# Kernel tuning notes

Hardware: AMD Instinct MI355X
Metric: run time of the kernel (lower is better)

Reference implementation:

```python
import jax, jax.numpy as jnp
import numpy as np

N_NODES = 50000
N_EDGES = 640000
DIM = 128
N_LAYERS = 4
K_MAX = 4


def setup_inputs() -> dict:
    key = jax.random.key(0)
    k1, k2, k3, k4, k5, k6 = jax.random.split(key, 6)
    x = jax.random.normal(k1, (N_NODES, DIM), dtype=jnp.float32)
    edge_index = jax.random.randint(k2, (2, N_EDGES), 0, N_NODES, dtype=jnp.int32)
    edge_attr = jax.random.randint(k3, (N_EDGES,), 1, K_MAX + 1, dtype=jnp.int32)  # hop k in [1, k_max]
    W = jax.random.normal(k4, (N_LAYERS, DIM, DIM), dtype=jnp.float32) * 0.05
    b = jax.random.normal(k5, (N_LAYERS, DIM), dtype=jnp.float32) * 0.01
    alpha = jax.random.normal(k6, (N_LAYERS, K_MAX), dtype=jnp.float32)
    return {"x": x, "edge_index": edge_index, "edge_attr": edge_attr,
            "W": W, "b": b, "alpha": alpha}


def reference(x, edge_index, edge_attr, W, b, alpha):
    # SP-GCN stage: per-hop GCN convs with shared per-layer weight W[t],
    # combined with softmax(alpha[t]) hop weights, residual + ReLU + L2 norm.
    N, D = x.shape
    L, K = alpha.shape
    src, dst = edge_index[0], edge_index[1]
    k_idx = edge_attr - 1                              # [E] in [0, K)

    # Per-(node, hop) in-degree with self-loop (+1), as in gcn_norm per k-subgraph.
    seg = dst * K + k_idx
    ones = jnp.ones(src.shape[0], dtype=x.dtype)
    deg = jax.ops.segment_sum(ones, seg, num_segments=N * K).reshape(N, K) + 1.0  # [N, K]
    dinv = jax.lax.rsqrt(deg)
    # symmetric norm per edge within its hop-k subgraph
    norm_e = dinv[src, k_idx] * dinv[dst, k_idx]       # [E]

    for t in range(L):
        a = jax.nn.softmax(alpha[t])                   # [K] hop weights
        h = x @ W[t]                                   # [N, D]
        # sum_k alpha_k * conv_k fused: per-edge weight alpha[k_e] * norm_e
        msg = (a[k_idx] * norm_e)[:, None] * h[src]    # [E, D]
        agg = jax.ops.segment_sum(msg, dst, num_segments=N)
        # self-loop contributions: sum_k alpha_k / deg[n, k]
        self_coef = jnp.sum(a[None, :] / deg, axis=1)  # [N]
        out = agg + self_coef[:, None] * h + b[t]
        x = x + jax.nn.relu(out)
        # F.normalize(p=2, dim=-1), eps=1e-12
        nrm = jnp.maximum(jnp.linalg.norm(x, axis=-1, keepdims=True), 1e-12)
        x = x / nrm
    return x
```

## Files before the change

### kernel.cpp

```cpp
#include <hip/hip_runtime.h>
#include <hip/hip_fp16.h>
#include <math.h>

#define DIM 128
#define KH 4

typedef unsigned int uint;
typedef unsigned short ushort;
using short8v = __attribute__((ext_vector_type(8))) short;
using f32x4 = __attribute__((ext_vector_type(4))) float;

__device__ __forceinline__ uint f2bf(float f) {
  uint u = __float_as_uint(f);
  return (u + 0x7fffu + ((u >> 16) & 1u)) >> 16;
}
__device__ __forceinline__ float bf2f(uint u) { return __uint_as_float(u << 16); }
__device__ __forceinline__ float bflo(uint u) { return __uint_as_float(u << 16); }
__device__ __forceinline__ float bfhi(uint u) { return __uint_as_float(u & 0xffff0000u); }

__global__ __launch_bounds__(256) void k_init_count(
    const float4* __restrict__ xin, float4* __restrict__ X4,
    uint* __restrict__ Xhi, uint* __restrict__ Xlo,
    const int* __restrict__ ei, const int* __restrict__ attr,
    uint* __restrict__ degpack, int n4, int E) {
  int i = blockIdx.x * 256 + threadIdx.x;
  if (i < n4) {
    float4 v = xin[i];
    X4[i] = v;
    uint h0 = f2bf(v.x), h1 = f2bf(v.y), h2 = f2bf(v.z), h3 = f2bf(v.w);
    Xhi[i * 2 + 0] = h0 | (h1 << 16);
    Xhi[i * 2 + 1] = h2 | (h3 << 16);
    uint l0 = f2bf(v.x - bf2f(h0)), l1 = f2bf(v.y - bf2f(h1));
    uint l2 = f2bf(v.z - bf2f(h2)), l3 = f2bf(v.w - bf2f(h3));
    Xlo[i * 2 + 0] = l0 | (l1 << 16);
    Xlo[i * 2 + 1] = l2 | (l3 << 16);
  }
  if (i < E) {
    int dst = ei[E + i];
    int k = attr[i] - 1;
    atomicAdd(&degpack[dst], 1u << (k * 8));
  }
}

__global__ __launch_bounds__(256) void k_scan1(const uint* __restrict__ degpack,
                                               int* __restrict__ off,
                                               int* __restrict__ bsum, int n) {
  __shared__ int s[256];
  int t = threadIdx.x;
  int i = blockIdx.x * 256 + t;
  int v = 0;
  if (i < n) {
    uint w = degpack[i];
    v = (w & 0xff) + ((w >> 8) & 0xff) + ((w >> 16) & 0xff) + (w >> 24);
  }
  s[t] = v;
  __syncthreads();
  for (int d = 1; d < 256; d <<= 1) {
    int u = (t >= d) ? s[t - d] : 0;
    __syncthreads();
    s[t] += u;
    __syncthreads();
  }
  if (i < n) off[i] = s[t] - v;
  if (t == 255) bsum[blockIdx.x] = s[255];
}

__global__ __launch_bounds__(256) void k_scan2(const int* __restrict__ bsum,
                                               int* __restrict__ bex, int nb) {
  __shared__ int s[256];
  int t = threadIdx.x;
  int v = (t < nb) ? bsum[t] : 0;
  s[t] = v;
  __syncthreads();
  for (int d = 1; d < 256; d <<= 1) {
    int u = (t >= d) ? s[t - d] : 0;
    __syncthreads();
    s[t] += u;
    __syncthreads();
  }
  if (t < nb) bex[t] = s[t] - v;
}

__global__ __launch_bounds__(256) void k_scan3w(int* __restrict__ off,
                                                const int* __restrict__ bex,
                                                const uint* __restrict__ degpack,
                                                int* __restrict__ cursor4,
                                                float* __restrict__ dinv, int n,
                                                const float* __restrict__ W,
                                                short* __restrict__ Whi,
                                                short* __restrict__ Wlo, int wtot) {
  int i = blockIdx.x * 256 + threadIdx.x;
  if (i < n) {
    int o = off[i] + bex[blockIdx.x];
    off[i] = o;
    uint w = degpack[i];
    int b0 = w & 0xff, b1 = (w >> 8) & 0xff, b2 = (w >> 16) & 0xff, b3 = w >> 24;
    int4 c;
    c.x = o;
    c.y = o + b0;
    c.z = o + b0 + b1;
    c.w = o + b0 + b1 + b2;
    *(int4*)&cursor4[i * 4] = c;
    float4 dv;
    dv.x = rsqrtf((float)b0 + 1.0f);
    dv.y = rsqrtf((float)b1 + 1.0f);
    dv.z = rsqrtf((float)b2 + 1.0f);
    dv.w = rsqrtf((float)b3 + 1.0f);
    *(float4*)&dinv[i * 4] = dv;
  }
  if (i < wtot) {
    int l = i >> 14;
    int rem = i & 16383;
    int k = rem >> 7;
    int ncol = rem & 127;
    float w = W[i];
    uint h = f2bf(w);
    uint lo = f2bf(w - bf2f(h));
    size_t o = (size_t)l * 16384 + (size_t)ncol * 128 + k;
    Whi[o] = (short)h;
    Wlo[o] = (short)lo;
  }
}

__global__ __launch_bounds__(256) void k_scatter(const int* __restrict__ ei,
                                                 const int* __restrict__ attr,
                                                 const float* __restrict__ dinv,
                                                 int* __restrict__ cursor4,
                                                 uint* __restrict__ srcnm, int E) {
  int e = blockIdx.x * 256 + threadIdx.x;
  if (e >= E) return;
  int src = ei[e];
  int dst = ei[E + e];
  int k = attr[e] - 1;
  float nm = dinv[src * KH + k] * dinv[dst * KH + k];
  ushort h = __half_as_ushort(__float2half(nm));
  int pos = atomicAdd(&cursor4[dst * KH + k], 1);
  srcnm[pos] = (uint)src | ((uint)h << 16);
}

__global__ __launch_bounds__(512) void k_gemm(const uint* __restrict__ Xhi,
                                              const uint* __restrict__ Xlo,
                                              const short* __restrict__ Whi,
                                              const short* __restrict__ Wlo,
                                              ushort* __restrict__ Hb16, int N) {
  __shared__ __align__(16) short xs_hi[64 * 128];
  __shared__ __align__(16) short xs_lo[64 * 128];
  int t = threadIdx.x;
  int r0 = blockIdx.x * 64;

#pragma unroll
  for (int i = 0; i < 2; ++i) {
    int fi = i * 512 + t;
    int row = fi >> 4, kq = fi & 15;
    int rg = r0 + row;
    if (rg >= N) rg = N - 1;
    int swz = kq ^ (row & 7);
    *(uint4*)&xs_hi[row * 128 + swz * 8] = *(const uint4*)&Xhi[(size_t)rg * 64 + kq * 4];
    *(uint4*)&xs_lo[row * 128 + swz * 8] = *(const uint4*)&Xlo[(size_t)rg * 64 + kq * 4];
  }
  __syncthreads();

  int wid = t >> 6, lane = t & 63;
  int wrow = wid & 1, wcol = wid >> 1;
  int lr = lane & 15, lk = lane >> 4;

  f32x4 acc[2][2];
#pragma unroll
  for (int a = 0; a < 2; ++a)
#pragma unroll
    for (int c = 0; c < 2; ++c) acc[a][c] = (f32x4){0.f, 0.f, 0.f, 0.f};

#pragma unroll
  for (int ks = 0; ks < 4; ++ks) {
    int k0 = ks * 32 + lk * 8;
    short8v ah[2], al[2];
#pragma unroll
    for (int rt = 0; rt < 2; ++rt) {
      int r = wrow * 32 + rt * 16 + lr;
      int slot = (k0 >> 3) ^ (r & 7);
      ah[rt] = *(short8v*)&xs_hi[r * 128 + slot * 8];
      al[rt] = *(short8v*)&xs_lo[r * 128 + slot * 8];
    }
    short8v bh[2], bl[2];
#pragma unroll
    for (int ct = 0; ct < 2; ++ct) {
      int col = wcol * 32 + ct * 16 + lr;
      bh[ct] = *(const short8v*)&Whi[(size_t)col * 128 + k0];
      bl[ct] = *(const short8v*)&Wlo[(size_t)col * 128 + k0];
    }
#pragma unroll
    for (int rt = 0; rt < 2; ++rt)
#pragma unroll
      for (int ct = 0; ct < 2; ++ct) {
        acc[rt][ct] = __builtin_amdgcn_mfma_f32_16x16x32_bf16(ah[rt], bh[ct], acc[rt][ct], 0, 0, 0);
        acc[rt][ct] = __builtin_amdgcn_mfma_f32_16x16x32_bf16(al[rt], bh[ct], acc[rt][ct], 0, 0, 0);
        acc[rt][ct] = __builtin_amdgcn_mfma_f32_16x16x32_bf16(ah[rt], bl[ct], acc[rt][ct], 0, 0, 0);
      }
  }

#pragma unroll
  for (int rt = 0; rt < 2; ++rt)
#pragma unroll
    for (int ct = 0; ct < 2; ++ct) {
      int col = wcol * 32 + ct * 16 + lr;
#pragma unroll
      for (int i = 0; i < 4; ++i) {
        int row = r0 + wrow * 32 + rt * 16 + lk * 4 + i;
        if (row < N) Hb16[(size_t)row * 128 + col] = (ushort)f2bf(acc[rt][ct][i]);
      }
    }
}

__global__ __launch_bounds__(256) void k_agg(const int* __restrict__ off,
                                             const uint* __restrict__ degpack,
                                             const uint* __restrict__ srcnm,
                                             const float* __restrict__ dinv,
                                             const uint* __restrict__ Hb,
                                             const float* __restrict__ bias,
                                             const float* __restrict__ alpha,
                                             float* __restrict__ X,
                                             uint* __restrict__ Xhi,
                                             uint* __restrict__ Xlo, int N) {
  int wid = threadIdx.x >> 6;
  int lane = threadIdx.x & 63;
  int n = blockIdx.x * 4 + wid;
  if (n >= N) return;

  float a0 = alpha[0], a1 = alpha[1], a2 = alpha[2], a3 = alpha[3];
  float m = fmaxf(fmaxf(a0, a1), fmaxf(a2, a3));
  a0 = __expf(a0 - m); a1 = __expf(a1 - m); a2 = __expf(a2 - m); a3 = __expf(a3 - m);
  float is = 1.0f / (a0 + a1 + a2 + a3);
  a0 *= is; a1 *= is; a2 *= is; a3 *= is;

  uint w = degpack[n];
  int b0 = w & 0xff, b1 = (w >> 8) & 0xff, b2 = (w >> 16) & 0xff, b3 = (int)(w >> 24);
  int e0 = off[n];
  int e1 = e0 + b0 + b1 + b2 + b3;
  int k1 = e0 + b0, k2 = k1 + b1, k3 = k2 + b2;

  float accx = 0.f, accy = 0.f;

  for (int base = e0; base < e1; base += 64) {
    int cnt = min(64, e1 - base);
    int sofs = 0;
    float wc = 0.f;
    if (lane < cnt) {
      uint v = srcnm[base + lane];
      int pos = base + lane;
      int k = (pos >= k1) + (pos >= k2) + (pos >= k3);
      float ak = (k == 0) ? a0 : (k == 1) ? a1 : (k == 2) ? a2 : a3;
      wc = ak * __half2float(__ushort_as_half((ushort)(v >> 16)));
      sofs = (int)(v & 0xFFFFu) << 6;
    }
    int j = 0;
    for (; j + 8 <= cnt; j += 8) {
      int s0 = __shfl(sofs, j),     s1 = __shfl(sofs, j + 1);
      int s2 = __shfl(sofs, j + 2), s3 = __shfl(sofs, j + 3);
      int s4 = __shfl(sofs, j + 4), s5 = __shfl(sofs, j + 5);
      int s6 = __shfl(sofs, j + 6), s7 = __shfl(sofs, j + 7);
      float w0 = __shfl(wc, j),     w1 = __shfl(wc, j + 1);
      float w2 = __shfl(wc, j + 2), w3 = __shfl(wc, j + 3);
      float w4 = __shfl(wc, j + 4), w5 = __shfl(wc, j + 5);
      float w6 = __shfl(wc, j + 6), w7 = __shfl(wc, j + 7);
      uint u0 = Hb[s0 + lane];
      uint u1 = Hb[s1 + lane];
      uint u2 = Hb[s2 + lane];
      uint u3 = Hb[s3 + lane];
      uint u4 = Hb[s4 + lane];
      uint u5 = Hb[s5 + lane];
      uint u6 = Hb[s6 + lane];
      uint u7 = Hb[s7 + lane];
      accx = fmaf(w0, bflo(u0), accx); accy = fmaf(w0, bfhi(u0), accy);
      accx = fmaf(w1, bflo(u1), accx); accy = fmaf(w1, bfhi(u1), accy);
      accx = fmaf(w2, bflo(u2), accx); accy = fmaf(w2, bfhi(u2), accy);
      accx = fmaf(w3, bflo(u3), accx); accy = fmaf(w3, bfhi(u3), accy);
      accx = fmaf(w4, bflo(u4), accx); accy = fmaf(w4, bfhi(u4), accy);
      accx = fmaf(w5, bflo(u5), accx); accy = fmaf(w5, bfhi(u5), accy);
      accx = fmaf(w6, bflo(u6), accx); accy = fmaf(w6, bfhi(u6), accy);
      accx = fmaf(w7, bflo(u7), accx); accy = fmaf(w7, bfhi(u7), accy);
    }
    for (; j + 4 <= cnt; j += 4) {
      int s0 = __shfl(sofs, j),     s1 = __shfl(sofs, j + 1);
      int s2 = __shfl(sofs, j + 2), s3 = __shfl(sofs, j + 3);
      float w0 = __shfl(wc, j),     w1 = __shfl(wc, j + 1);
      float w2 = __shfl(wc, j + 2), w3 = __shfl(wc, j + 3);
      uint u0 = Hb[s0 + lane];
      uint u1 = Hb[s1 + lane];
      uint u2 = Hb[s2 + lane];
      uint u3 = Hb[s3 + lane];
      accx = fmaf(w0, bflo(u0), accx); accy = fmaf(w0, bfhi(u0), accy);
      accx = fmaf(w1, bflo(u1), accx); accy = fmaf(w1, bfhi(u1), accy);
      accx = fmaf(w2, bflo(u2), accx); accy = fmaf(w2, bfhi(u2), accy);
      accx = fmaf(w3, bflo(u3), accx); accy = fmaf(w3, bfhi(u3), accy);
    }
    for (; j < cnt; ++j) {
      int sj = __shfl(sofs, j);
      float wj = __shfl(wc, j);
      uint uj = Hb[sj + lane];
      accx = fmaf(wj, bflo(uj), accx);
      accy = fmaf(wj, bfhi(uj), accy);
    }
  }

  float4 dv = *(const float4*)&dinv[n * 4];
  float sc = a0 * dv.x * dv.x + a1 * dv.y * dv.y + a2 * dv.z * dv.z + a3 * dv.w * dv.w;

  uint un = Hb[(size_t)n * 64 + lane];
  float2 bb = ((const float2*)bias)[lane];
  float2 xo = ((const float2*)X)[(size_t)n * 64 + lane];
  float o0 = accx + sc * bflo(un) + bb.x;
  float o1 = accy + sc * bfhi(un) + bb.y;
  float x0 = xo.x + fmaxf(o0, 0.f);
  float x1 = xo.y + fmaxf(o1, 0.f);

  float ss = x0 * x0 + x1 * x1;
#pragma unroll
  for (int d = 32; d; d >>= 1) ss += __shfl_xor(ss, d);
  float nrm = fmaxf(sqrtf(ss), 1e-12f);
  float inv = 1.0f / nrm;
  float y0 = x0 * inv, y1 = x1 * inv;
  ((float2*)X)[(size_t)n * 64 + lane] = make_float2(y0, y1);

  uint h0 = f2bf(y0), h1 = f2bf(y1);
  Xhi[(size_t)n * 64 + lane] = h0 | (h1 << 16);
  uint l0 = f2bf(y0 - bf2f(h0)), l1 = f2bf(y1 - bf2f(h1));
  Xlo[(size_t)n * 64 + lane] = l0 | (l1 << 16);
}

extern "C" void kernel_launch(void* const* d_in, const int* in_sizes, int n_in,
                              void* d_out, int out_size, void* d_ws, size_t ws_size,
                              hipStream_t stream) {
  const float* x = (const float*)d_in[0];
  const int* ei = (const int*)d_in[1];
  const int* attr = (const int*)d_in[2];
  const float* W = (const float*)d_in[3];
  const float* b = (const float*)d_in[4];
  const float* alpha = (const float*)d_in[5];
  float* X = (float*)d_out;

  int N = in_sizes[0] / DIM;
  int E = in_sizes[1] / 2;
  int L = in_sizes[3] / (DIM * DIM);

  char* base = (char*)d_ws;
  size_t ofs = 0;
  auto carve = [&](size_t bytes) -> void* {
    void* p = base + ofs;
    ofs = (ofs + bytes + 255) & ~(size_t)255;
    return p;
  };
  int* off = (int*)carve((size_t)(N + 1) * 4);
  int* cursor4 = (int*)carve((size_t)N * KH * 4);
  uint* degpack = (uint*)carve((size_t)N * 4);
  float* dinv = (float*)carve((size_t)N * KH * 4);
  int* bsum = (int*)carve(256 * 4);
  int* bex = (int*)carve(256 * 4);
  uint* srcnm = (uint*)carve((size_t)E * 4);
  uint* Hb = (uint*)carve((size_t)N * 64 * 4);
  uint* Xhi = (uint*)carve((size_t)N * 64 * 4);
  uint* Xlo = (uint*)carve((size_t)N * 64 * 4);
  short* Whi = (short*)carve((size_t)L * DIM * DIM * 2);
  short* Wlo = (short*)carve((size_t)L * DIM * DIM * 2);

  int n4 = N * DIM / 4;
  int nb = (N + 255) / 256;
  int wtot = L * DIM * DIM;
  int gmax = (wtot > N) ? wtot : N;

  hipMemsetAsync(degpack, 0, (size_t)N * 4, stream);
  k_init_count<<<(n4 + 255) / 256, 256, 0, stream>>>((const float4*)x, (float4*)X,
                                                     Xhi, Xlo, ei, attr, degpack,
                                                     n4, E);
  k_scan1<<<nb, 256, 0, stream>>>(degpack, off, bsum, N);
  k_scan2<<<1, 256, 0, stream>>>(bsum, bex, nb);
  k_scan3w<<<(gmax + 255) / 256, 256, 0, stream>>>(off, bex, degpack, cursor4, dinv, N,
                                                   W, Whi, Wlo, wtot);
  k_scatter<<<(E + 255) / 256, 256, 0, stream>>>(ei, attr, dinv, cursor4, srcnm, E);

  for (int t = 0; t < L; ++t) {
    k_gemm<<<(N + 63) / 64, 512, 0, stream>>>(Xhi, Xlo,
                                              Whi + (size_t)t * DIM * DIM,
                                              Wlo + (size_t)t * DIM * DIM,
                                              (ushort*)Hb, N);
    k_agg<<<(N + 3) / 4, 256, 0, stream>>>(off, degpack, srcnm, dinv, Hb,
                                           b + (size_t)t * DIM, alpha + (size_t)t * KH,
                                           X, Xhi, Xlo, N);
  }
}
```

Baseline: 316.6 us.

## Slice H by feature columns and aggregate per slice for cache locality

Stores the GEMM output H in four column slices of 32 features and splits aggregation into slice-major blocks, so each pass gathers from a smaller, cache-resident slice. Each wave processes four edges at once with 16 lanes per edge and reduces across lane groups. The residual, ReLU and normalization move into a separate post kernel that reads an fp32 aggregation buffer. This trades more edge-list reads, an extra buffer round trip and an extra launch for better gather locality.

```diff
diff --git a/kernel.cpp b/kernel.cpp
--- a/kernel.cpp
+++ b/kernel.cpp
@@ -203,27 +203,30 @@
 #pragma unroll
     for (int ct = 0; ct < 2; ++ct) {
       int col = wcol * 32 + ct * 16 + lr;
+      int slice = col >> 5, cw = col & 31;
 #pragma unroll
       for (int i = 0; i < 4; ++i) {
         int row = r0 + wrow * 32 + rt * 16 + lk * 4 + i;
-        if (row < N) Hb16[(size_t)row * 128 + col] = (ushort)f2bf(acc[rt][ct][i]);
+        if (row < N)
+          Hb16[(size_t)slice * N * 32 + (size_t)row * 32 + cw] = (ushort)f2bf(acc[rt][ct][i]);
       }
     }
 }
 
-__global__ __launch_bounds__(256) void k_agg(const int* __restrict__ off,
-                                             const uint* __restrict__ degpack,
-                                             const uint* __restrict__ srcnm,
-                                             const float* __restrict__ dinv,
-                                             const uint* __restrict__ Hb,
-                                             const float* __restrict__ bias,
-                                             const float* __restrict__ alpha,
-                                             float* __restrict__ X,
-                                             uint* __restrict__ Xhi,
-                                             uint* __restrict__ Xlo, int N) {
+__global__ __launch_bounds__(256) void k_aggs(const int* __restrict__ off,
+                                              const uint* __restrict__ degpack,
+                                              const uint* __restrict__ srcnm,
+                                              const float* __restrict__ dinv,
+                                              const uint* __restrict__ Hb,
+                                              const float* __restrict__ alpha,
+                                              float2* __restrict__ agg,
+                                              int N, int nbx) {
+  int bid = blockIdx.x;
+  int slice = bid / nbx;
+  int nodeblk = bid - slice * nbx;
   int wid = threadIdx.x >> 6;
   int lane = threadIdx.x & 63;
-  int n = blockIdx.x * 4 + wid;
+  int n = nodeblk * 4 + wid;
   if (n >= N) return;
 
   float a0 = alpha[0], a1 = alpha[1], a2 = alpha[2], a3 = alpha[3];
@@ -237,6 +240,10 @@
   int e0 = off[n];
   int e1 = e0 + b0 + b1 + b2 + b3;
   int k1 = e0 + b0, k2 = k1 + b1, k3 = k2 + b2;
+
+  const uint* Hs = Hb + (size_t)slice * N * 16;
+  int g = lane >> 4;
+  int cl = lane & 15;
 
   float accx = 0.f, accy = 0.f;
 
@@ -250,74 +257,54 @@
       int k = (pos >= k1) + (pos >= k2) + (pos >= k3);
       float ak = (k == 0) ? a0 : (k == 1) ? a1 : (k == 2) ? a2 : a3;
       wc = ak * __half2float(__ushort_as_half((ushort)(v >> 16)));
-      sofs = (int)(v & 0xFFFFu) << 6;
-    }
-    int j = 0;
-    for (; j + 8 <= cnt; j += 8) {
-      int s0 = __shfl(sofs, j),     s1 = __shfl(sofs, j + 1);
-      int s2 = __shfl(sofs, j + 2), s3 = __shfl(sofs, j + 3);
-      int s4 = __shfl(sofs, j + 4), s5 = __shfl(sofs, j + 5);
-      int s6 = __shfl(sofs, j + 6), s7 = __shfl(sofs, j + 7);
-      float w0 = __shfl(wc, j),     w1 = __shfl(wc, j + 1);
-      float w2 = __shfl(wc, j + 2), w3 = __shfl(wc, j + 3);
-      float w4 = __shfl(wc, j + 4), w5 = __shfl(wc, j + 5);
-      float w6 = __shfl(wc, j + 6), w7 = __shfl(wc, j + 7);
-      uint u0 = Hb[s0 + lane];
-      uint u1 = Hb[s1 + lane];
-      uint u2 = Hb[s2 + lane];
-      uint u3 = Hb[s3 + lane];
-      uint u4 = Hb[s4 + lane];
-      uint u5 = Hb[s5 + lane];
-      uint u6 = Hb[s6 + lane];
-      uint u7 = Hb[s7 + lane];
-      accx = fmaf(w0, bflo(u0), accx); accy = fmaf(w0, bfhi(u0), accy);
-      accx = fmaf(w1, bflo(u1), accx); accy = fmaf(w1, bfhi(u1), accy);
-      accx = fmaf(w2, bflo(u2), accx); accy = fmaf(w2, bfhi(u2), accy);
-      accx = fmaf(w3, bflo(u3), accx); accy = fmaf(w3, bfhi(u3), accy);
-      accx = fmaf(w4, bflo(u4), accx); accy = fmaf(w4, bfhi(u4), accy);
-      accx = fmaf(w5, bflo(u5), accx); accy = fmaf(w5, bfhi(u5), accy);
-      accx = fmaf(w6, bflo(u6), accx); accy = fmaf(w6, bfhi(u6), accy);
-      accx = fmaf(w7, bflo(u7), accx); accy = fmaf(w7, bfhi(u7), accy);
-    }
-    for (; j + 4 <= cnt; j += 4) {
-      int s0 = __shfl(sofs, j),     s1 = __shfl(sofs, j + 1);
-      int s2 = __shfl(sofs, j + 2), s3 = __shfl(sofs, j + 3);
-      float w0 = __shfl(wc, j),     w1 = __shfl(wc, j + 1);
-      float w2 = __shfl(wc, j + 2), w3 = __shfl(wc, j + 3);
-      uint u0 = Hb[s0 + lane];
-      uint u1 = Hb[s1 + lane];
-      uint u2 = Hb[s2 + lane];
-      uint u3 = Hb[s3 + lane];
-      accx = fmaf(w0, bflo(u0), accx); accy = fmaf(w0, bfhi(u0), accy);
-      accx = fmaf(w1, bflo(u1), accx); accy = fmaf(w1, bfhi(u1), accy);
-      accx = fmaf(w2, bflo(u2), accx); accy = fmaf(w2, bfhi(u2), accy);
-      accx = fmaf(w3, bflo(u3), accx); accy = fmaf(w3, bfhi(u3), accy);
-    }
-    for (; j < cnt; ++j) {
-      int sj = __shfl(sofs, j);
-      float wj = __shfl(wc, j);
-      uint uj = Hb[sj + lane];
-      accx = fmaf(wj, bflo(uj), accx);
-      accy = fmaf(wj, bfhi(uj), accy);
-    }
-  }
-
-  float4 dv = *(const float4*)&dinv[n * 4];
-  float sc = a0 * dv.x * dv.x + a1 * dv.y * dv.y + a2 * dv.z * dv.z + a3 * dv.w * dv.w;
-
-  uint un = Hb[(size_t)n * 64 + lane];
+      sofs = (int)(v & 0xFFFFu) << 4;
+    }
+    int jmax = (cnt + 3) >> 2;
+    for (int j = 0; j < jmax; ++j) {
+      int idx = j * 4 + g;
+      int sj = __shfl(sofs, idx);
+      float wj = __shfl(wc, idx);
+      uint u = Hs[sj + cl];
+      accx = fmaf(wj, bflo(u), accx);
+      accy = fmaf(wj, bfhi(u), accy);
+    }
+  }
+
+  accx += __shfl_xor(accx, 16);
+  accx += __shfl_xor(accx, 32);
+  accy += __shfl_xor(accy, 16);
+  accy += __shfl_xor(accy, 32);
+
+  if (g == 0) {
+    float4 dv = *(const float4*)&dinv[n * 4];
+    float sc = a0 * dv.x * dv.x + a1 * dv.y * dv.y + a2 * dv.z * dv.z + a3 * dv.w * dv.w;
+    uint un = Hs[(size_t)n * 16 + cl];
+    accx = fmaf(sc, bflo(un), accx);
+    accy = fmaf(sc, bfhi(un), accy);
+    agg[(size_t)n * 64 + slice * 16 + cl] = make_float2(accx, accy);
+  }
+}
+
+__global__ __launch_bounds__(256) void k_post(const float2* __restrict__ agg,
+                                              const float* __restrict__ bias,
+                                              float* __restrict__ X,
+                                              uint* __restrict__ Xhi,
+                                              uint* __restrict__ Xlo, int N) {
+  int wid = threadIdx.x >> 6;
+  int lane = threadIdx.x & 63;
+  int n = blockIdx.x * 4 + wid;
+  if (n >= N) return;
+
+  float2 o = agg[(size_t)n * 64 + lane];
   float2 bb = ((const float2*)bias)[lane];
   float2 xo = ((const float2*)X)[(size_t)n * 64 + lane];
-  float o0 = accx + sc * bflo(un) + bb.x;
-  float o1 = accy + sc * bfhi(un) + bb.y;
-  float x0 = xo.x + fmaxf(o0, 0.f);
-  float x1 = xo.y + fmaxf(o1, 0.f);
+  float x0 = xo.x + fmaxf(o.x + bb.x, 0.f);
+  float x1 = xo.y + fmaxf(o.y + bb.y, 0.f);
 
   float ss = x0 * x0 + x1 * x1;
 #pragma unroll
   for (int d = 32; d; d >>= 1) ss += __shfl_xor(ss, d);
-  float nrm = fmaxf(sqrtf(ss), 1e-12f);
-  float inv = 1.0f / nrm;
+  float inv = 1.0f / fmaxf(sqrtf(ss), 1e-12f);
   float y0 = x0 * inv, y1 = x1 * inv;
   ((float2*)X)[(size_t)n * 64 + lane] = make_float2(y0, y1);
 
@@ -359,6 +346,7 @@
   uint* Hb = (uint*)carve((size_t)N * 64 * 4);
   uint* Xhi = (uint*)carve((size_t)N * 64 * 4);
   uint* Xlo = (uint*)carve((size_t)N * 64 * 4);
+  float2* agg = (float2*)carve((size_t)N * 64 * 8);
   short* Whi = (short*)carve((size_t)L * DIM * DIM * 2);
   short* Wlo = (short*)carve((size_t)L * DIM * DIM * 2);
 
@@ -366,6 +354,7 @@
   int nb = (N + 255) / 256;
   int wtot = L * DIM * DIM;
   int gmax = (wtot > N) ? wtot : N;
+  int nbx = (N + 3) / 4;
 
   hipMemsetAsync(degpack, 0, (size_t)N * 4, stream);
   k_init_count<<<(n4 + 255) / 256, 256, 0, stream>>>((const float4*)x, (float4*)X,
@@ -382,8 +371,8 @@
                                               Whi + (size_t)t * DIM * DIM,
                                               Wlo + (size_t)t * DIM * DIM,
                                               (ushort*)Hb, N);
-    k_agg<<<(N + 3) / 4, 256, 0, stream>>>(off, degpack, srcnm, dinv, Hb,
-                                           b + (size_t)t * DIM, alpha + (size_t)t * KH,
-                                           X, Xhi, Xlo, N);
-  }
-}
+    k_aggs<<<nbx * 4, 256, 0, stream>>>(off, degpack, srcnm, dinv, Hb,
+                                        alpha + (size_t)t * KH, agg, N, nbx);
+    k_post<<<nbx, 256, 0, stream>>>(agg, b + (size_t)t * DIM, X, Xhi, Xlo, N);
+  }
+}
```

Result: slower. 539.5 us (+70.4%).

## Partition degree-count and CSR scatter atomics by destination range across block groups

Applied to the files above, without the earlier changes.

Splits edge degree counting out of the init kernel and rewrites both the count and scatter kernels so each of 8 block groups handles only destinations in one eighth of the node range. Blocks in the same group scan a slice of edges and perform atomics only on matching destinations. The intent is to keep each group's atomic targets in a smaller region, likely to improve cache or L2 locality and reduce atomic contention spread. In exchange every edge's dst index is read 8 times and an extra kernel launch is added.

```diff
diff --git a/kernel.cpp b/kernel.cpp
--- a/kernel.cpp
+++ b/kernel.cpp
@@ -18,11 +18,9 @@
 __device__ __forceinline__ float bflo(uint u) { return __uint_as_float(u << 16); }
 __device__ __forceinline__ float bfhi(uint u) { return __uint_as_float(u & 0xffff0000u); }
 
-__global__ __launch_bounds__(256) void k_init_count(
+__global__ __launch_bounds__(256) void k_init(
     const float4* __restrict__ xin, float4* __restrict__ X4,
-    uint* __restrict__ Xhi, uint* __restrict__ Xlo,
-    const int* __restrict__ ei, const int* __restrict__ attr,
-    uint* __restrict__ degpack, int n4, int E) {
+    uint* __restrict__ Xhi, uint* __restrict__ Xlo, int n4) {
   int i = blockIdx.x * 256 + threadIdx.x;
   if (i < n4) {
     float4 v = xin[i];
@@ -35,10 +33,25 @@
     Xlo[i * 2 + 0] = l0 | (l1 << 16);
     Xlo[i * 2 + 1] = l2 | (l3 << 16);
   }
-  if (i < E) {
-    int dst = ei[E + i];
-    int k = attr[i] - 1;
-    atomicAdd(&degpack[dst], 1u << (k * 8));
+}
+
+__global__ __launch_bounds__(256) void k_countg(const int* __restrict__ ei,
+                                                const int* __restrict__ attr,
+                                                uint* __restrict__ degpack,
+                                                int E, int N, int bpg) {
+  int g = blockIdx.x & 7;
+  int l = blockIdx.x >> 3;
+  int lo = (int)(((long long)N * g) >> 3);
+  int hi = (int)(((long long)N * (g + 1)) >> 3);
+  int per = (E + bpg - 1) / bpg;
+  int e0 = l * per;
+  int e1 = min(E, e0 + per);
+  for (int e = e0 + threadIdx.x; e < e1; e += 256) {
+    int dst = ei[E + e];
+    if (dst >= lo && dst < hi) {
+      int k = attr[e] - 1;
+      atomicAdd(&degpack[dst], 1u << (k * 8));
+    }
   }
 }
 
@@ -122,20 +135,30 @@
   }
 }
 
-__global__ __launch_bounds__(256) void k_scatter(const int* __restrict__ ei,
-                                                 const int* __restrict__ attr,
-                                                 const float* __restrict__ dinv,
-                                                 int* __restrict__ cursor4,
-                                                 uint* __restrict__ srcnm, int E) {
-  int e = blockIdx.x * 256 + threadIdx.x;
-  if (e >= E) return;
-  int src = ei[e];
-  int dst = ei[E + e];
-  int k = attr[e] - 1;
-  float nm = dinv[src * KH + k] * dinv[dst * KH + k];
-  ushort h = __half_as_ushort(__float2half(nm));
-  int pos = atomicAdd(&cursor4[dst * KH + k], 1);
-  srcnm[pos] = (uint)src | ((uint)h << 16);
+__global__ __launch_bounds__(256) void k_scatterg(const int* __restrict__ ei,
+                                                  const int* __restrict__ attr,
+                                                  const float* __restrict__ dinv,
+                                                  int* __restrict__ cursor4,
+                                                  uint* __restrict__ srcnm,
+                                                  int E, int N, int bpg) {
+  int g = blockIdx.x & 7;
+  int l = blockIdx.x >> 3;
+  int lo = (int)(((long long)N * g) >> 3);
+  int hi = (int)(((long long)N * (g + 1)) >> 3);
+  int per = (E + bpg - 1) / bpg;
+  int e0 = l * per;
+  int e1 = min(E, e0 + per);
+  for (int e = e0 + threadIdx.x; e < e1; e += 256) {
+    int dst = ei[E + e];
+    if (dst >= lo && dst < hi) {
+      int src = ei[e];
+      int k = attr[e] - 1;
+      float nm = dinv[src * KH + k] * dinv[dst * KH + k];
+      ushort h = __half_as_ushort(__float2half(nm));
+      int pos = atomicAdd(&cursor4[dst * KH + k], 1);
+      srcnm[pos] = (uint)src | ((uint)h << 16);
+    }
+  }
 }
 
 __global__ __launch_bounds__(512) void k_gemm(const uint* __restrict__ Xhi,
@@ -366,16 +389,17 @@
   int nb = (N + 255) / 256;
   int wtot = L * DIM * DIM;
   int gmax = (wtot > N) ? wtot : N;
+  int bpg = 256;
 
   hipMemsetAsync(degpack, 0, (size_t)N * 4, stream);
-  k_init_count<<<(n4 + 255) / 256, 256, 0, stream>>>((const float4*)x, (float4*)X,
-                                                     Xhi, Xlo, ei, attr, degpack,
-                                                     n4, E);
+  k_init<<<(n4 + 255) / 256, 256, 0, stream>>>((const float4*)x, (float4*)X,
+                                               Xhi, Xlo, n4);
+  k_countg<<<8 * bpg, 256, 0, stream>>>(ei, attr, degpack, E, N, bpg);
   k_scan1<<<nb, 256, 0, stream>>>(degpack, off, bsum, N);
   k_scan2<<<1, 256, 0, stream>>>(bsum, bex, nb);
   k_scan3w<<<(gmax + 255) / 256, 256, 0, stream>>>(off, bex, degpack, cursor4, dinv, N,
                                                    W, Whi, Wlo, wtot);
-  k_scatter<<<(E + 255) / 256, 256, 0, stream>>>(ei, attr, dinv, cursor4, srcnm, E);
+  k_scatterg<<<8 * bpg, 256, 0, stream>>>(ei, attr, dinv, cursor4, srcnm, E, N, bpg);
 
   for (int t = 0; t < L; ++t) {
     k_gemm<<<(N + 63) / 64, 512, 0, stream>>>(Xhi, Xlo,
```

Result: no change. 320.6 us (+1.3%).
